# Kernel tuning notes

Measured on AMD Instinct MI355X. Metric: run time of the kernel, lower is better.

The kernel has to match this reference:

```python
import jax, jax.numpy as jnp
import numpy as np
from jax.experimental.jet import jet

ORDER = 3  # Taylor order from init_kwargs
D, C, H = 4096, 4096, 8192


def setup_inputs() -> dict:
    key = jax.random.key(0)
    k = jax.random.split(key, 6)
    sc1 = 1.0 / np.sqrt(D + C)
    sc2 = 1.0 / np.sqrt(H)
    return {
        "h": jax.random.normal(k[0], (D,), jnp.float32),
        "r": jnp.zeros((), jnp.float32),  # ignored residual slot of h_r tuple
        "t": jax.random.uniform(k[1], (), jnp.float32),
        "c": jax.random.normal(k[2], (C,), jnp.float32),
        "W1": jax.random.normal(k[3], (D + C, H), jnp.float32) * sc1,
        "b1": jnp.zeros((H,), jnp.float32),
        "W2": jax.random.normal(k[4], (H, D), jnp.float32) * sc2,
        "b2": jnp.zeros((D,), jnp.float32),
    }


def reference(h, r, t, c, W1, b1, W2, b2):
    # dynamics f(h, t, c): 2-layer tanh MLP on concat(h, c)
    def f(_h, _t, _c):
        x = jnp.concatenate((_h, _c))
        return jnp.tanh(x @ W1 + b1) @ W2 + b2

    h_shape = h.shape

    def g(h_t):
        # expand flattened state+time through dynamics
        _h, _t = jnp.reshape(h_t[:-1], h_shape), h_t[-1]
        dh = jnp.ravel(f(_h, _t, c))
        return jnp.concatenate((dh, jnp.array([1.0], dtype=dh.dtype)))

    h_t = jnp.concatenate((jnp.ravel(h), jnp.reshape(t, (1,))))
    # recursive Taylor-mode jet expansion
    (y0, [*yns]) = jet(g, (h_t,), ((jnp.ones_like(h_t),),))
    for _ in range(ORDER - 1):
        (y0, [*yns]) = jet(g, (h_t,), ((y0, *yns),))
    dydt = jnp.reshape(y0[:-1], h_shape)
    drdt = jnp.reshape(yns[-2][:-1], h_shape)
    return (dydt, jnp.mean(drdt ** 2))
```

## Files before the change

kernel.cpp:

```cpp
#include <hip/hip_runtime.h>

#define DD 4096
#define HH 8192

enum Stage { S_X0 = 0, S_TANH, S_BIASOUT, S_PMUL, S_COPY, S_S2 };

typedef float vfloat4 __attribute__((ext_vector_type(4)));

__device__ inline unsigned short f2bf(float f) {
    unsigned int u = __float_as_uint(f);
    u += 0x7FFFu + ((u >> 16) & 1u);
    return (unsigned short)(u >> 16);
}

template <bool NT, bool CONV, int KS, int NTOT>
__device__ inline void stream_f32(const float* __restrict__ Wp,
                                  const float* __restrict__ xs,
                                  float* __restrict__ op,
                                  unsigned short* __restrict__ Wbp) {
    float ax = 0.f, ay = 0.f, az = 0.f, aw = 0.f;
#pragma unroll 8
    for (int k = 0; k < KS; ++k) {
        const float xv = xs[k];
        const float* row = Wp + (size_t)k * NTOT;
        vfloat4 w;
        if constexpr (NT)
            w = __builtin_nontemporal_load(reinterpret_cast<const vfloat4*>(row));
        else
            w = *reinterpret_cast<const vfloat4*>(row);
        ax = fmaf(xv, w.x, ax);
        ay = fmaf(xv, w.y, ay);
        az = fmaf(xv, w.z, az);
        aw = fmaf(xv, w.w, aw);
        if constexpr (CONV) {
            ushort4 o;
            o.x = f2bf(w.x); o.y = f2bf(w.y); o.z = f2bf(w.z); o.w = f2bf(w.w);
            *reinterpret_cast<ushort4*>(Wbp + (size_t)k * NTOT) = o;
        }
    }
    *reinterpret_cast<float4*>(op) = make_float4(ax, ay, az, aw);
}

template <int STAGE, int KS, int SPREV, int KPREV>
__device__ inline void prologue(const float* __restrict__ Pprev,
                                const float* __restrict__ h, const float* __restrict__ c,
                                const float* __restrict__ b1, const float* __restrict__ b2,
                                float* __restrict__ s0g, float* __restrict__ t0g,
                                float* __restrict__ a1g, float* __restrict__ outv,
                                float* xs, float* part, int k0, int bx)
{
    constexpr int GROUPS = 256 / KS;
    const int tid = threadIdx.x;
    if constexpr (STAGE == S_X0) {
        if (tid < KS) {
            int k = k0 + tid;
            xs[tid] = (k < DD) ? h[k] : c[k - DD];
        }
    } else {
        const int g = tid / KS, j = tid % KS;
        float acc = 0.f;
        for (int s = g; s < SPREV; s += GROUPS)
            acc += Pprev[(size_t)s * KPREV + k0 + j];
        part[g * KS + j] = acc;
        __syncthreads();
        if (tid < KS) {
            const int k = k0 + tid;
            float tot = 0.f;
#pragma unroll
            for (int g2 = 0; g2 < GROUPS; ++g2) tot += part[g2 * KS + tid];
            float xv;
            if constexpr (STAGE == S_TANH) {
                float s = tanhf(tot + b1[k]);
                xv = s;
                if (bx == 0) { s0g[k] = s; t0g[k] = 1.f - s * s; }
            } else if constexpr (STAGE == S_BIASOUT) {
                xv = tot + b2[k];
                if (bx == 0) outv[k] = xv;
            } else if constexpr (STAGE == S_PMUL) {
                xv = t0g[k] * tot;
                if (bx == 0) a1g[k] = tot;
            } else if constexpr (STAGE == S_COPY) {
                xv = tot;
            } else {
                float a1v = a1g[k];
                xv = t0g[k] * (tot - s0g[k] * a1v * a1v);
            }
            xs[tid] = xv;
        }
    }
    __syncthreads();
}

template <int STAGE, int KS, int SPREV, int KPREV, int NTOT, int NTMODE, bool CONV>
__global__ __launch_bounds__(256) void gemv_f32(
    const float* __restrict__ W, const float* __restrict__ Pprev,
    float* __restrict__ Pout, unsigned short* __restrict__ Wb,
    const float* __restrict__ h, const float* __restrict__ c,
    const float* __restrict__ b1, const float* __restrict__ b2,
    float* __restrict__ s0g, float* __restrict__ t0g, float* __restrict__ a1g,
    float* __restrict__ outv, unsigned* __restrict__ ctrz)
{
    __shared__ float xs[KS];
    __shared__ float part[256];
    const int bx = blockIdx.x, by = blockIdx.y;
    const int k0 = by * KS;
    prologue<STAGE, KS, SPREV, KPREV>(Pprev, h, c, b1, b2, s0g, t0g, a1g, outv,
                                      xs, part, k0, bx);

    if constexpr (STAGE == S_S2) {
        if (bx == 0 && by == 0 && threadIdx.x == 0) *ctrz = 0u;
    }

    const int ncol = bx * 1024 + threadIdx.x * 4;
    const float* Wp = W + (size_t)k0 * NTOT + ncol;
    float* op = Pout + (size_t)by * NTOT + ncol;
    unsigned short* Wbp = CONV ? (Wb + (size_t)k0 * NTOT + ncol) : nullptr;

    if constexpr (NTMODE == 0) {
        stream_f32<false, false, KS, NTOT>(Wp, xs, op, nullptr);
    } else if constexpr (NTMODE == 1) {
        stream_f32<true, false, KS, NTOT>(Wp, xs, op, nullptr);
    } else {
        if (k0 >= DD) stream_f32<true, false, KS, NTOT>(Wp, xs, op, nullptr);
        else          stream_f32<false, CONV, KS, NTOT>(Wp, xs, op, Wbp);
    }
}

template <int STAGE, int KS, int SPREV, int KPREV, int NTOT>
__global__ __launch_bounds__(256) void gemv_b16(
    const unsigned short* __restrict__ Wb, const float* __restrict__ Pprev,
    float* __restrict__ Pout,
    const float* __restrict__ h, const float* __restrict__ c,
    const float* __restrict__ b1, const float* __restrict__ b2,
    float* __restrict__ s0g, float* __restrict__ t0g, float* __restrict__ a1g,
    float* __restrict__ outv)
{
    __shared__ float xs[KS];
    __shared__ float part[256];
    const int bx = blockIdx.x, by = blockIdx.y;
    const int k0 = by * KS;
    prologue<STAGE, KS, SPREV, KPREV>(Pprev, h, c, b1, b2, s0g, t0g, a1g, outv,
                                      xs, part, k0, bx);

    const int ncol = bx * 2048 + threadIdx.x * 8;
    const unsigned short* Wp = Wb + (size_t)k0 * NTOT + ncol;
    float a0 = 0.f, a1 = 0.f, a2 = 0.f, a3 = 0.f;
    float a4 = 0.f, a5 = 0.f, a6 = 0.f, a7 = 0.f;
#pragma unroll 8
    for (int k = 0; k < KS; ++k) {
        const float xv = xs[k];
        const uint4 w = *reinterpret_cast<const uint4*>(Wp + (size_t)k * NTOT);
        a0 = fmaf(xv, __uint_as_float(w.x << 16), a0);
        a1 = fmaf(xv, __uint_as_float(w.x & 0xFFFF0000u), a1);
        a2 = fmaf(xv, __uint_as_float(w.y << 16), a2);
        a3 = fmaf(xv, __uint_as_float(w.y & 0xFFFF0000u), a3);
        a4 = fmaf(xv, __uint_as_float(w.z << 16), a4);
        a5 = fmaf(xv, __uint_as_float(w.z & 0xFFFF0000u), a5);
        a6 = fmaf(xv, __uint_as_float(w.w << 16), a6);
        a7 = fmaf(xv, __uint_as_float(w.w & 0xFFFF0000u), a7);
    }
    float* op = Pout + (size_t)by * NTOT + ncol;
    *reinterpret_cast<float4*>(op)     = make_float4(a0, a1, a2, a3);
    *reinterpret_cast<float4*>(op + 4) = make_float4(a4, a5, a6, a7);
}

template <int SPREV>
__global__ __launch_bounds__(256) void reduce_sq_final(const float* __restrict__ P6,
                                                       float* __restrict__ psum,
                                                       unsigned* __restrict__ ctr,
                                                       float* __restrict__ dout) {
    const int n = blockIdx.x * 256 + threadIdx.x;
    float acc = 0.f;
#pragma unroll 8
    for (int s = 0; s < SPREV; ++s) acc += P6[(size_t)s * DD + n];
    float sq = acc * acc;
    for (int off = 32; off; off >>= 1) sq += __shfl_down(sq, off);
    __shared__ float ls[4];
    const int wid = threadIdx.x >> 6;
    if ((threadIdx.x & 63) == 0) ls[wid] = sq;
    __syncthreads();
    if (threadIdx.x == 0) {
        psum[blockIdx.x] = ls[0] + ls[1] + ls[2] + ls[3];
        __threadfence();
        unsigned old = atomicAdd(ctr, 1u);
        if (old == 15u) {
            __threadfence();
            float t = 0.f;
#pragma unroll
            for (int i = 0; i < 16; ++i) t += psum[i];
            dout[DD] = t / (float)DD;
        }
    }
}

extern "C" void kernel_launch(void* const* d_in, const int* in_sizes, int n_in,
                              void* d_out, int out_size, void* d_ws, size_t ws_size,
                              hipStream_t stream) {
    const float* h  = (const float*)d_in[0];
    const float* c  = (const float*)d_in[3];
    const float* W1 = (const float*)d_in[4];
    const float* b1 = (const float*)d_in[5];
    const float* W2 = (const float*)d_in[6];
    const float* b2 = (const float*)d_in[7];
    float* out = (float*)d_out;
    float* ws = (float*)d_ws;

    float* P1 = ws;
    float* P2 = P1 + 1048576;
    float* P3 = P2 + 1048576;
    float* P4 = P3 + 2097152;
    float* P5 = P4 + 1048576;
    float* P6 = P5 + 2097152;
    float* s0 = P6 + 1048576;
    float* t0 = s0 + 8192;
    float* a1 = t0 + 8192;
    float* psum = a1 + 8192;
    unsigned* ctr = (unsigned*)(psum + 16);
    unsigned short* W1b = (unsigned short*)(psum + 64);

    gemv_f32<S_X0, 64, 1, 1, HH, 2, true><<<dim3(8, 128), 256, 0, stream>>>(
        W1, nullptr, P1, W1b, h, c, b1, b2, s0, t0, a1, out, nullptr);
    gemv_f32<S_TANH, 32, 128, HH, DD, 0, false><<<dim3(4, 256), 256, 0, stream>>>(
        W2, P1, P2, nullptr, h, c, b1, b2, s0, t0, a1, out, nullptr);
    gemv_b16<S_BIASOUT, 16, 256, DD, HH><<<dim3(4, 256), 256, 0, stream>>>(
        W1b, P2, P3, h, c, b1, b2, s0, t0, a1, out);
    gemv_f32<S_PMUL, 32, 256, HH, DD, 0, false><<<dim3(4, 256), 256, 0, stream>>>(
        W2, P3, P4, nullptr, h, c, b1, b2, s0, t0, a1, out, nullptr);
    gemv_b16<S_COPY, 16, 256, DD, HH><<<dim3(4, 256), 256, 0, stream>>>(
        W1b, P4, P5, h, c, b1, b2, s0, t0, a1, out);
    gemv_f32<S_S2, 32, 256, HH, DD, 1, false><<<dim3(4, 256), 256, 0, stream>>>(
        W2, P5, P6, nullptr, h, c, b1, b2, s0, t0, a1, out, ctr);
    reduce_sq_final<256><<<16, 256, 0, stream>>>(P6, psum, ctr, out);
}
```

Baseline: 202.5 us.

## Split split-K partial reduction into separate reduce kernels between GEMV stages

Moves the split-K partial-sum reduction and elementwise activation out of each GEMV prologue into dedicated reduce_x kernels that write a compact x vector. Before, every GEMV block redundantly re-read and summed all partials for its K slice (each K slice was reduced once per column block, so 4-8x redundant traffic). Now each partial column is reduced exactly once, and GEMV blocks just load their KS inputs. This adds five extra kernel launches and their serialization overhead. The final square-reduction is also widened to 64 blocks.

```diff
diff --git a/kernel.cpp b/kernel.cpp
--- a/kernel.cpp
+++ b/kernel.cpp
@@ -3,7 +3,7 @@
 #define DD 4096
 #define HH 8192
 
-enum Stage { S_X0 = 0, S_TANH, S_BIASOUT, S_PMUL, S_COPY, S_S2 };
+enum Stage { S_TANH = 1, S_BIASOUT, S_PMUL, S_COPY, S_S2 };
 
 typedef float vfloat4 __attribute__((ext_vector_type(4)));
 
@@ -13,136 +13,147 @@
     return (unsigned short)(u >> 16);
 }
 
-template <bool NT, bool CONV, int KS, int NTOT>
-__device__ inline void stream_f32(const float* __restrict__ Wp,
-                                  const float* __restrict__ xs,
-                                  float* __restrict__ op,
-                                  unsigned short* __restrict__ Wbp) {
+template <int KS>
+__global__ __launch_bounds__(256) void gemv_p1(
+    const float* __restrict__ W1, float* __restrict__ Pout,
+    unsigned short* __restrict__ Wb,
+    const float* __restrict__ h, const float* __restrict__ c)
+{
+    __shared__ float xs[KS];
+    const int tid = threadIdx.x, bx = blockIdx.x, by = blockIdx.y;
+    const int k0 = by * KS;
+    if (tid < KS) {
+        int k = k0 + tid;
+        xs[tid] = (k < DD) ? h[k] : c[k - DD];
+    }
+    __syncthreads();
+
+    const int ncol = bx * 1024 + tid * 4;
+    const float* Wp = W1 + (size_t)k0 * HH + ncol;
+    float* op = Pout + (size_t)by * HH + ncol;
+    float ax = 0.f, ay = 0.f, az = 0.f, aw = 0.f;
+
+    if (k0 < DD) {
+        unsigned short* Wbp = Wb + (size_t)k0 * HH + ncol;
+#pragma unroll 8
+        for (int k = 0; k < KS; ++k) {
+            const float xv = xs[k];
+            const vfloat4 w = *reinterpret_cast<const vfloat4*>(Wp + (size_t)k * HH);
+            ax = fmaf(xv, w.x, ax);
+            ay = fmaf(xv, w.y, ay);
+            az = fmaf(xv, w.z, az);
+            aw = fmaf(xv, w.w, aw);
+            ushort4 o;
+            o.x = f2bf(w.x); o.y = f2bf(w.y); o.z = f2bf(w.z); o.w = f2bf(w.w);
+            *reinterpret_cast<ushort4*>(Wbp + (size_t)k * HH) = o;
+        }
+    } else {
+#pragma unroll 8
+        for (int k = 0; k < KS; ++k) {
+            const float xv = xs[k];
+            const vfloat4 w = __builtin_nontemporal_load(
+                reinterpret_cast<const vfloat4*>(Wp + (size_t)k * HH));
+            ax = fmaf(xv, w.x, ax);
+            ay = fmaf(xv, w.y, ay);
+            az = fmaf(xv, w.z, az);
+            aw = fmaf(xv, w.w, aw);
+        }
+    }
+    *reinterpret_cast<float4*>(op) = make_float4(ax, ay, az, aw);
+}
+
+template <int STAGE, int SPREV, int KPREV>
+__global__ __launch_bounds__(256) void reduce_x(
+    const float* __restrict__ Pprev, float* __restrict__ xg,
+    const float* __restrict__ b1, const float* __restrict__ b2,
+    float* __restrict__ s0g, float* __restrict__ t0g, float* __restrict__ a1g,
+    float* __restrict__ outv, unsigned* __restrict__ ctr)
+{
+    __shared__ float part[256];
+    const int tid = threadIdx.x;
+    const int col = blockIdx.x * 64 + (tid & 63);
+    const int sg = tid >> 6;
+
+    if constexpr (STAGE == S_S2) {
+        if (blockIdx.x == 0 && tid == 0) *ctr = 0u;
+    }
+
+    float acc = 0.f;
+#pragma unroll 8
+    for (int s = sg; s < SPREV; s += 4)
+        acc += Pprev[(size_t)s * KPREV + col];
+    part[tid] = acc;
+    __syncthreads();
+
+    if (tid < 64) {
+        const int n = blockIdx.x * 64 + tid;
+        float tot = part[tid] + part[tid + 64] + part[tid + 128] + part[tid + 192];
+        float xv;
+        if constexpr (STAGE == S_TANH) {
+            float sv = tanhf(tot + b1[n]);
+            s0g[n] = sv;
+            t0g[n] = 1.f - sv * sv;
+            xv = sv;
+        } else if constexpr (STAGE == S_BIASOUT) {
+            xv = tot + b2[n];
+            outv[n] = xv;
+        } else if constexpr (STAGE == S_PMUL) {
+            a1g[n] = tot;
+            xv = t0g[n] * tot;
+        } else if constexpr (STAGE == S_COPY) {
+            xv = tot;
+        } else {
+            float a1v = a1g[n];
+            xv = t0g[n] * (tot - s0g[n] * a1v * a1v);
+        }
+        xg[n] = xv;
+    }
+}
+
+template <int KS, int NTOT, bool NT>
+__global__ __launch_bounds__(256) void gemv_f32x(
+    const float* __restrict__ W, const float* __restrict__ xg,
+    float* __restrict__ Pout)
+{
+    __shared__ float xs[KS];
+    const int tid = threadIdx.x, bx = blockIdx.x, by = blockIdx.y;
+    const int k0 = by * KS;
+    if (tid < KS) xs[tid] = xg[k0 + tid];
+    __syncthreads();
+
+    const int ncol = bx * 1024 + tid * 4;
+    const float* Wp = W + (size_t)k0 * NTOT + ncol;
     float ax = 0.f, ay = 0.f, az = 0.f, aw = 0.f;
 #pragma unroll 8
     for (int k = 0; k < KS; ++k) {
         const float xv = xs[k];
-        const float* row = Wp + (size_t)k * NTOT;
         vfloat4 w;
         if constexpr (NT)
-            w = __builtin_nontemporal_load(reinterpret_cast<const vfloat4*>(row));
+            w = __builtin_nontemporal_load(
+                reinterpret_cast<const vfloat4*>(Wp + (size_t)k * NTOT));
         else
-            w = *reinterpret_cast<const vfloat4*>(row);
+            w = *reinterpret_cast<const vfloat4*>(Wp + (size_t)k * NTOT);
         ax = fmaf(xv, w.x, ax);
         ay = fmaf(xv, w.y, ay);
         az = fmaf(xv, w.z, az);
         aw = fmaf(xv, w.w, aw);
-        if constexpr (CONV) {
-            ushort4 o;
-            o.x = f2bf(w.x); o.y = f2bf(w.y); o.z = f2bf(w.z); o.w = f2bf(w.w);
-            *reinterpret_cast<ushort4*>(Wbp + (size_t)k * NTOT) = o;
-        }
-    }
-    *reinterpret_cast<float4*>(op) = make_float4(ax, ay, az, aw);
-}
-
-template <int STAGE, int KS, int SPREV, int KPREV>
-__device__ inline void prologue(const float* __restrict__ Pprev,
-                                const float* __restrict__ h, const float* __restrict__ c,
-                                const float* __restrict__ b1, const float* __restrict__ b2,
-                                float* __restrict__ s0g, float* __restrict__ t0g,
-                                float* __restrict__ a1g, float* __restrict__ outv,
-                                float* xs, float* part, int k0, int bx)
-{
-    constexpr int GROUPS = 256 / KS;
-    const int tid = threadIdx.x;
-    if constexpr (STAGE == S_X0) {
-        if (tid < KS) {
-            int k = k0 + tid;
-            xs[tid] = (k < DD) ? h[k] : c[k - DD];
-        }
-    } else {
-        const int g = tid / KS, j = tid % KS;
-        float acc = 0.f;
-        for (int s = g; s < SPREV; s += GROUPS)
-            acc += Pprev[(size_t)s * KPREV + k0 + j];
-        part[g * KS + j] = acc;
-        __syncthreads();
-        if (tid < KS) {
-            const int k = k0 + tid;
-            float tot = 0.f;
-#pragma unroll
-            for (int g2 = 0; g2 < GROUPS; ++g2) tot += part[g2 * KS + tid];
-            float xv;
-            if constexpr (STAGE == S_TANH) {
-                float s = tanhf(tot + b1[k]);
-                xv = s;
-                if (bx == 0) { s0g[k] = s; t0g[k] = 1.f - s * s; }
-            } else if constexpr (STAGE == S_BIASOUT) {
-                xv = tot + b2[k];
-                if (bx == 0) outv[k] = xv;
-            } else if constexpr (STAGE == S_PMUL) {
-                xv = t0g[k] * tot;
-                if (bx == 0) a1g[k] = tot;
-            } else if constexpr (STAGE == S_COPY) {
-                xv = tot;
-            } else {
-                float a1v = a1g[k];
-                xv = t0g[k] * (tot - s0g[k] * a1v * a1v);
-            }
-            xs[tid] = xv;
-        }
-    }
-    __syncthreads();
-}
-
-template <int STAGE, int KS, int SPREV, int KPREV, int NTOT, int NTMODE, bool CONV>
-__global__ __launch_bounds__(256) void gemv_f32(
-    const float* __restrict__ W, const float* __restrict__ Pprev,
-    float* __restrict__ Pout, unsigned short* __restrict__ Wb,
-    const float* __restrict__ h, const float* __restrict__ c,
-    const float* __restrict__ b1, const float* __restrict__ b2,
-    float* __restrict__ s0g, float* __restrict__ t0g, float* __restrict__ a1g,
-    float* __restrict__ outv, unsigned* __restrict__ ctrz)
+    }
+    *reinterpret_cast<float4*>(Pout + (size_t)by * NTOT + ncol) =
+        make_float4(ax, ay, az, aw);
+}
+
+template <int KS, int NTOT>
+__global__ __launch_bounds__(256) void gemv_b16x(
+    const unsigned short* __restrict__ Wb, const float* __restrict__ xg,
+    float* __restrict__ Pout)
 {
     __shared__ float xs[KS];
-    __shared__ float part[256];
-    const int bx = blockIdx.x, by = blockIdx.y;
+    const int tid = threadIdx.x, bx = blockIdx.x, by = blockIdx.y;
     const int k0 = by * KS;
-    prologue<STAGE, KS, SPREV, KPREV>(Pprev, h, c, b1, b2, s0g, t0g, a1g, outv,
-                                      xs, part, k0, bx);
-
-    if constexpr (STAGE == S_S2) {
-        if (bx == 0 && by == 0 && threadIdx.x == 0) *ctrz = 0u;
-    }
-
-    const int ncol = bx * 1024 + threadIdx.x * 4;
-    const float* Wp = W + (size_t)k0 * NTOT + ncol;
-    float* op = Pout + (size_t)by * NTOT + ncol;
-    unsigned short* Wbp = CONV ? (Wb + (size_t)k0 * NTOT + ncol) : nullptr;
-
-    if constexpr (NTMODE == 0) {
-        stream_f32<false, false, KS, NTOT>(Wp, xs, op, nullptr);
-    } else if constexpr (NTMODE == 1) {
-        stream_f32<true, false, KS, NTOT>(Wp, xs, op, nullptr);
-    } else {
-        if (k0 >= DD) stream_f32<true, false, KS, NTOT>(Wp, xs, op, nullptr);
-        else          stream_f32<false, CONV, KS, NTOT>(Wp, xs, op, Wbp);
-    }
-}
-
-template <int STAGE, int KS, int SPREV, int KPREV, int NTOT>
-__global__ __launch_bounds__(256) void gemv_b16(
-    const unsigned short* __restrict__ Wb, const float* __restrict__ Pprev,
-    float* __restrict__ Pout,
-    const float* __restrict__ h, const float* __restrict__ c,
-    const float* __restrict__ b1, const float* __restrict__ b2,
-    float* __restrict__ s0g, float* __restrict__ t0g, float* __restrict__ a1g,
-    float* __restrict__ outv)
-{
-    __shared__ float xs[KS];
-    __shared__ float part[256];
-    const int bx = blockIdx.x, by = blockIdx.y;
-    const int k0 = by * KS;
-    prologue<STAGE, KS, SPREV, KPREV>(Pprev, h, c, b1, b2, s0g, t0g, a1g, outv,
-                                      xs, part, k0, bx);
-
-    const int ncol = bx * 2048 + threadIdx.x * 8;
+    if (tid < KS) xs[tid] = xg[k0 + tid];
+    __syncthreads();
+
+    const int ncol = bx * 2048 + tid * 8;
     const unsigned short* Wp = Wb + (size_t)k0 * NTOT + ncol;
     float a0 = 0.f, a1 = 0.f, a2 = 0.f, a3 = 0.f;
     float a4 = 0.f, a5 = 0.f, a6 = 0.f, a7 = 0.f;
@@ -165,30 +176,37 @@
 }
 
 template <int SPREV>
-__global__ __launch_bounds__(256) void reduce_sq_final(const float* __restrict__ P6,
-                                                       float* __restrict__ psum,
-                                                       unsigned* __restrict__ ctr,
-                                                       float* __restrict__ dout) {
-    const int n = blockIdx.x * 256 + threadIdx.x;
+__global__ __launch_bounds__(256) void reduce_sq_final(
+    const float* __restrict__ P6, float* __restrict__ psum,
+    unsigned* __restrict__ ctr, float* __restrict__ dout)
+{
+    __shared__ float part[256];
+    const int tid = threadIdx.x;
+    const int col = blockIdx.x * 64 + (tid & 63);
+    const int sg = tid >> 6;
+
     float acc = 0.f;
 #pragma unroll 8
-    for (int s = 0; s < SPREV; ++s) acc += P6[(size_t)s * DD + n];
-    float sq = acc * acc;
-    for (int off = 32; off; off >>= 1) sq += __shfl_down(sq, off);
-    __shared__ float ls[4];
-    const int wid = threadIdx.x >> 6;
-    if ((threadIdx.x & 63) == 0) ls[wid] = sq;
-    __syncthreads();
-    if (threadIdx.x == 0) {
-        psum[blockIdx.x] = ls[0] + ls[1] + ls[2] + ls[3];
-        __threadfence();
-        unsigned old = atomicAdd(ctr, 1u);
-        if (old == 15u) {
+    for (int s = sg; s < SPREV; s += 4)
+        acc += P6[(size_t)s * DD + col];
+    part[tid] = acc;
+    __syncthreads();
+
+    if (tid < 64) {
+        float tot = part[tid] + part[tid + 64] + part[tid + 128] + part[tid + 192];
+        float sq = tot * tot;
+        for (int off = 32; off; off >>= 1) sq += __shfl_down(sq, off);
+        if (tid == 0) {
+            psum[blockIdx.x] = sq;
             __threadfence();
-            float t = 0.f;
+            unsigned old = atomicAdd(ctr, 1u);
+            if (old == 63u) {
+                __threadfence();
+                float t = 0.f;
 #pragma unroll
-            for (int i = 0; i < 16; ++i) t += psum[i];
-            dout[DD] = t / (float)DD;
+                for (int i = 0; i < 64; ++i) t += psum[i];
+                dout[DD] = t / (float)DD;
+            }
         }
     }
 }
@@ -214,21 +232,30 @@
     float* s0 = P6 + 1048576;
     float* t0 = s0 + 8192;
     float* a1 = t0 + 8192;
-    float* psum = a1 + 8192;
-    unsigned* ctr = (unsigned*)(psum + 16);
-    unsigned short* W1b = (unsigned short*)(psum + 64);
-
-    gemv_f32<S_X0, 64, 1, 1, HH, 2, true><<<dim3(8, 128), 256, 0, stream>>>(
-        W1, nullptr, P1, W1b, h, c, b1, b2, s0, t0, a1, out, nullptr);
-    gemv_f32<S_TANH, 32, 128, HH, DD, 0, false><<<dim3(4, 256), 256, 0, stream>>>(
-        W2, P1, P2, nullptr, h, c, b1, b2, s0, t0, a1, out, nullptr);
-    gemv_b16<S_BIASOUT, 16, 256, DD, HH><<<dim3(4, 256), 256, 0, stream>>>(
-        W1b, P2, P3, h, c, b1, b2, s0, t0, a1, out);
-    gemv_f32<S_PMUL, 32, 256, HH, DD, 0, false><<<dim3(4, 256), 256, 0, stream>>>(
-        W2, P3, P4, nullptr, h, c, b1, b2, s0, t0, a1, out, nullptr);
-    gemv_b16<S_COPY, 16, 256, DD, HH><<<dim3(4, 256), 256, 0, stream>>>(
-        W1b, P4, P5, h, c, b1, b2, s0, t0, a1, out);
-    gemv_f32<S_S2, 32, 256, HH, DD, 1, false><<<dim3(4, 256), 256, 0, stream>>>(
-        W2, P5, P6, nullptr, h, c, b1, b2, s0, t0, a1, out, ctr);
-    reduce_sq_final<256><<<16, 256, 0, stream>>>(P6, psum, ctr, out);
-}
+    float* x2 = a1 + 8192;
+    float* x3 = x2 + 8192;
+    float* x4 = x3 + 4096;
+    float* x5 = x4 + 8192;
+    float* x6 = x5 + 4096;
+    float* psum = x6 + 8192;
+    unsigned* ctr = (unsigned*)(psum + 64);
+    unsigned short* W1b = (unsigned short*)(psum + 128);
+
+    gemv_p1<64><<<dim3(8, 128), 256, 0, stream>>>(W1, P1, W1b, h, c);
+    reduce_x<S_TANH, 128, HH><<<128, 256, 0, stream>>>(
+        P1, x2, b1, b2, s0, t0, a1, out, ctr);
+    gemv_f32x<32, DD, false><<<dim3(4, 256), 256, 0, stream>>>(W2, x2, P2);
+    reduce_x<S_BIASOUT, 256, DD><<<64, 256, 0, stream>>>(
+        P2, x3, b1, b2, s0, t0, a1, out, ctr);
+    gemv_b16x<16, HH><<<dim3(4, 256), 256, 0, stream>>>(W1b, x3, P3);
+    reduce_x<S_PMUL, 256, HH><<<128, 256, 0, stream>>>(
+        P3, x4, b1, b2, s0, t0, a1, out, ctr);
+    gemv_f32x<32, DD, false><<<dim3(4, 256), 256, 0, stream>>>(W2, x4, P4);
+    reduce_x<S_COPY, 256, DD><<<64, 256, 0, stream>>>(
+        P4, x5, b1, b2, s0, t0, a1, out, ctr);
+    gemv_b16x<16, HH><<<dim3(4, 256), 256, 0, stream>>>(W1b, x5, P5);
+    reduce_x<S_S2, 256, HH><<<128, 256, 0, stream>>>(
+        P5, x6, b1, b2, s0, t0, a1, out, ctr);
+    gemv_f32x<32, DD, true><<<dim3(4, 256), 256, 0, stream>>>(W2, x6, P6);
+    reduce_sq_final<256><<<64, 256, 0, stream>>>(P6, psum, ctr, out);
+}
```

Measured after the change: 202.4 us. No clear change (-0.1%).
